# Kernel tuning notes

Measured on AMD Instinct MI355X. Metric: run time of the kernel, lower is better.

Reference implementation:

```python
import jax, jax.numpy as jnp
import numpy as np

H = 32        # query heads
KVH = 8       # key/value heads
D = 64        # head_dim
HID = 2048
B, S = 2, 2048

def rotate_half(x):
    x1, x2 = x[..., :D // 2], x[..., D // 2:]
    return jnp.concatenate((-x2, x1), axis=-1)

def setup_inputs() -> dict:
    key = jax.random.key(0)
    ks = jax.random.split(key, 7)
    scale = 1.0 / np.sqrt(HID)
    return {
        "x": jax.random.normal(ks[0], (B, S, HID), jnp.float32),
        "cos": jax.random.uniform(ks[1], (S, D), jnp.float32),
        "sin": jax.random.uniform(ks[2], (S, D), jnp.float32),
        "wq": jax.random.normal(ks[3], (HID, H * D), jnp.float32) * scale,
        "wk": jax.random.normal(ks[4], (HID, KVH * D), jnp.float32) * scale,
        "wv": jax.random.normal(ks[5], (HID, KVH * D), jnp.float32) * scale,
        "wo": jax.random.normal(ks[6], (HID, HID), jnp.float32) * scale,
    }

def reference(x, cos, sin, wq, wk, wv, wo):
    b, s, _ = x.shape
    # QKV projections -> [b, heads, s, d]
    q = (x @ wq).reshape(b, s, H, D).transpose(0, 2, 1, 3)
    k = (x @ wk).reshape(b, s, KVH, D).transpose(0, 2, 1, 3)
    v = (x @ wv).reshape(b, s, KVH, D).transpose(0, 2, 1, 3)
    # RoPE (cos/sin broadcast over batch and heads)
    c = cos[None, None, :, :]
    si = sin[None, None, :, :]
    q = q * c + rotate_half(q) * si
    k = k * c + rotate_half(k) * si
    # GQA: expand kv heads (repeat_interleave on head axis)
    g = H // KVH
    k = jnp.repeat(k, g, axis=1)
    v = jnp.repeat(v, g, axis=1)
    # causal SDPA
    scores = jnp.einsum("bhqd,bhkd->bhqk", q, k) / np.sqrt(D).astype(np.float32)
    causal = jnp.tril(jnp.ones((s, s), dtype=bool))
    scores = jnp.where(causal[None, None], scores, jnp.finfo(scores.dtype).min)
    attn = jax.nn.softmax(scores, axis=-1)
    out = jnp.einsum("bhqk,bhkd->bhqd", attn, v)
    out = out.transpose(0, 2, 1, 3).reshape(b, s, H * D)
    return out @ wo
```

## Files before the change

kernel.cpp:

```cpp
#include <hip/hip_runtime.h>
#include <stdint.h>

#define B_ 2
#define S_ 2048
#define H_ 32
#define KVH_ 8
#define D_ 64
#define HID_ 2048

typedef float f32x4 __attribute__((ext_vector_type(4)));
typedef float f32x16 __attribute__((ext_vector_type(16)));
typedef short bf16x8 __attribute__((ext_vector_type(8)));
typedef unsigned short u16;
typedef unsigned short u16x4 __attribute__((ext_vector_type(4)));
typedef unsigned short u16x8 __attribute__((ext_vector_type(8)));
typedef unsigned int u32;
typedef unsigned int u32x2 __attribute__((ext_vector_type(2)));
typedef unsigned int u32x4 __attribute__((ext_vector_type(4)));

__device__ __forceinline__ u16 f2b(float f) {
  unsigned u = __builtin_bit_cast(unsigned, f);
  u += 0x7fffu + ((u >> 16) & 1u);
  return (u16)(u >> 16);
}
__device__ __forceinline__ float b2f(u16 h) {
  unsigned u = ((unsigned)h) << 16;
  return __builtin_bit_cast(float, u);
}
__device__ __forceinline__ void gl_lds16(const void* g, void* l) {
  __builtin_amdgcn_global_load_lds(
      (const __attribute__((address_space(1))) unsigned*)g,
      (__attribute__((address_space(3))) unsigned*)l, 16, 0, 0);
}
__device__ __forceinline__ f32x4 mfma16(bf16x8 a, bf16x8 b, f32x4 c) {
  return __builtin_amdgcn_mfma_f32_16x16x32_bf16(a, b, c, 0, 0, 0);
}
__device__ __forceinline__ f32x16 mfma32(bf16x8 a, bf16x8 b, f32x16 c) {
  return __builtin_amdgcn_mfma_f32_32x32x16_bf16(a, b, c, 0, 0, 0);
}
__device__ __forceinline__ u32 cvtpk(float lo, float hi) {
  u32 r;
  asm("v_cvt_pk_bf16_f32 %0, %1, %2" : "=v"(r) : "v"(lo), "v"(hi));
  return r;
}
__device__ __forceinline__ float fast_exp2(float x) {
#if __has_builtin(__builtin_amdgcn_exp2f)
  return __builtin_amdgcn_exp2f(x);
#else
  return exp2f(x);
#endif
}
__device__ __forceinline__ void swap32(u32 a, u32 b, u32& x, u32& y) {
#if __has_builtin(__builtin_amdgcn_permlane32_swap)
  auto r = __builtin_amdgcn_permlane32_swap(a, b, false, false);
  x = r[0];
  y = r[1];
#else
  u32 sa = (u32)__shfl_xor((int)a, 32), sb = (u32)__shfl_xor((int)b, 32);
  bool hib = (threadIdx.x & 32) != 0;
  x = hib ? sb : a;
  y = hib ? b : sa;
#endif
}

__global__ __launch_bounds__(256) void k_cvt(const float* __restrict__ src,
                                             u16* __restrict__ dst, int n4) {
  int i = blockIdx.x * 256 + threadIdx.x;
  if (i >= n4) return;
  f32x4 v = *(const f32x4*)(src + (size_t)i * 4);
  u16x4 o;
  o[0] = f2b(v[0]); o[1] = f2b(v[1]); o[2] = f2b(v[2]); o[3] = f2b(v[3]);
  *(u16x4*)(dst + (size_t)i * 4) = o;
}

__global__ __launch_bounds__(256) void k_transpose4(const float* __restrict__ wq,
                                                    const float* __restrict__ wk,
                                                    const float* __restrict__ wv,
                                                    const float* __restrict__ wo,
                                                    u16* __restrict__ wqkvT,
                                                    u16* __restrict__ woT) {
  __shared__ float t[32][33];
  const int K = 2048;
  int bx = blockIdx.x;
  const float* src;
  u16* dst;
  int N, n0;
  if (bx < 64) {
    src = wq; dst = wqkvT; N = 2048; n0 = bx * 32;
  } else if (bx < 80) {
    src = wk; dst = wqkvT + (size_t)2048 * 2048; N = 512; n0 = (bx - 64) * 32;
  } else if (bx < 96) {
    src = wv; dst = wqkvT + (size_t)2560 * 2048; N = 512; n0 = (bx - 80) * 32;
  } else {
    src = wo; dst = woT; N = 2048; n0 = (bx - 96) * 32;
  }
  int k0 = blockIdx.y * 32;
  int tt = threadIdx.x;
  int r = tt >> 3, c4 = (tt & 7) << 2;
  f32x4 v = *(const f32x4*)(src + (size_t)(k0 + r) * N + n0 + c4);
  t[r][c4 + 0] = v[0]; t[r][c4 + 1] = v[1];
  t[r][c4 + 2] = v[2]; t[r][c4 + 3] = v[3];
  __syncthreads();
  u16x4 o;
  o[0] = f2b(t[c4 + 0][r]); o[1] = f2b(t[c4 + 1][r]);
  o[2] = f2b(t[c4 + 2][r]); o[3] = f2b(t[c4 + 3][r]);
  *(u16x4*)(dst + (size_t)(n0 + r) * K + k0 + c4) = o;
}

__device__ __forceinline__ void stage64(const u16* __restrict__ G, int rowbase,
                                        int K, int kt, u16* unit, int tid) {
  int r = tid >> 3, sl = tid & 7;
  gl_lds16(G + (size_t)(rowbase + r) * K + kt * 64 + ((sl ^ (r & 7)) << 3),
           (char*)unit + tid * 16);
}

template <int BN, int OUTF32>
__global__ __launch_bounds__(512, 1) void k_gemm8(const u16* __restrict__ A,
                                                  const u16* __restrict__ BT,
                                                  float* __restrict__ Cf,
                                                  u16* __restrict__ Cb,
                                                  int M, int N, int K) {
  constexpr int ATILE = 256 * 64;
  constexpr int BTILE = BN * 64;
  constexpr int BU = BN / 64;
  constexpr int WN = (BN == 128) ? 2 : 4;
  constexpr int NI = (BN == 192) ? 3 : 4;
  constexpr int MI = (BN == 128) ? 4 : 8;
  constexpr int MIP = MI / 4;
  __shared__ __align__(16) u16 sm[2 * ATILE + 2 * BTILE];
  const int tid = threadIdx.x;
  const int l = tid & 63;
  const int lg = (l >> 4) & 3, lr = l & 15;
  const int w = tid >> 6;
  const int wm = w / WN, wn = w % WN;

  const int nwg = gridDim.x;
  const int cpx = nwg >> 3;
  const int bid = blockIdx.x;
  const int swz = (bid & 7) * cpx + (bid >> 3);
  const int ntn = N / BN;
  const int bm = swz / ntn, bn = swz % ntn;
  const int m0 = bm << 8, n0 = bn * BN;

  const u16* Ag = A + (size_t)m0 * K;
  const u16* Bg = BT + (size_t)n0 * K;
  u16* As = sm;
  u16* Bs = sm + 2 * ATILE;

  const int nt = K >> 6;
  f32x4 acc[MI][NI] = {};

#pragma unroll
  for (int u = 0; u < 4; ++u) stage64(Ag, u * 64, K, 0, As + u * 4096, tid);
#pragma unroll
  for (int u = 0; u < BU; ++u) stage64(Bg, u * 64, K, 0, Bs + u * 4096, tid);
  stage64(Ag, 0, K, 1, As + ATILE, tid);
  stage64(Ag, 64, K, 1, As + ATILE + 4096, tid);
  asm volatile("s_waitcnt vmcnt(2)" ::: "memory");
  __builtin_amdgcn_s_barrier();
  asm volatile("" ::: "memory");

  for (int t = 0; t < nt; ++t) {
    const int cur = t & 1;
    u16* Ac = As + cur * ATILE;
    u16* Bc = Bs + cur * BTILE;
    u16* An = As + (cur ^ 1) * ATILE;
    u16* Bn = Bs + (cur ^ 1) * BTILE;
    bf16x8 bc[NI][2];
#pragma unroll
    for (int q = 0; q < 4; ++q) {
      bf16x8 af[MIP][2];
#pragma unroll
      for (int mi2 = 0; mi2 < MIP; ++mi2)
#pragma unroll
        for (int ks = 0; ks < 2; ++ks) {
          int row = wm * (MI * 16) + (q * MIP + mi2) * 16 + lr;
          int slot = (ks * 4 + lg) ^ (lr & 7);
          af[mi2][ks] = *(const bf16x8*)&Ac[row * 64 + slot * 8];
        }
      if (q == 0) {
#pragma unroll
        for (int ni = 0; ni < NI; ++ni)
#pragma unroll
          for (int ks = 0; ks < 2; ++ks) {
            int row = wn * (NI * 16) + ni * 16 + lr;
            int slot = (ks * 4 + lg) ^ (lr & 7);
            bc[ni][ks] = *(const bf16x8*)&Bc[row * 64 + slot * 8];
          }
      }
      if (t + 1 < nt) {
        if (q == 0) {
          stage64(Ag, 128, K, t + 1, An + 2 * 4096, tid);
          stage64(Ag, 192, K, t + 1, An + 3 * 4096, tid);
        } else if (q == 1) {
          stage64(Bg, 0, K, t + 1, Bn, tid);
          stage64(Bg, 64, K, t + 1, Bn + 4096, tid);
        } else if (q == 2) {
          if (BU >= 3) stage64(Bg, 128, K, t + 1, Bn + 2 * 4096, tid);
          if (BU >= 4) stage64(Bg, 192, K, t + 1, Bn + 3 * 4096, tid);
        }
      }
      __builtin_amdgcn_s_barrier();
      asm volatile("" ::: "memory");
      __builtin_amdgcn_s_setprio(1);
#pragma unroll
      for (int mi2 = 0; mi2 < MIP; ++mi2)
#pragma unroll
        for (int ni = 0; ni < NI; ++ni)
#pragma unroll
          for (int ks = 0; ks < 2; ++ks)
            acc[q * MIP + mi2][ni] =
                mfma16(af[mi2][ks], bc[ni][ks], acc[q * MIP + mi2][ni]);
      __builtin_amdgcn_s_setprio(0);
      if (q == 3) {
        if (t + 2 < nt) {
          stage64(Ag, 0, K, t + 2, Ac, tid);
          stage64(Ag, 64, K, t + 2, Ac + 4096, tid);
          asm volatile("s_waitcnt vmcnt(2)" ::: "memory");
        } else if (t + 1 < nt) {
          asm volatile("s_waitcnt vmcnt(0)" ::: "memory");
        }
      }
      __builtin_amdgcn_s_barrier();
      asm volatile("" ::: "memory");
    }
  }

#pragma unroll
  for (int mi = 0; mi < MI; ++mi)
#pragma unroll
    for (int ni = 0; ni < NI; ++ni)
#pragma unroll
      for (int j = 0; j < 4; ++j) {
        size_t row = (size_t)m0 + wm * (MI * 16) + mi * 16 + lg * 4 + j;
        size_t col = (size_t)n0 + wn * (NI * 16) + ni * 16 + lr;
        if (OUTF32)
          Cf[row * N + col] = acc[mi][ni][j];
        else
          Cb[row * N + col] = f2b(acc[mi][ni][j]);
      }
}

__global__ __launch_bounds__(256) void k_rope(const u16* __restrict__ qkv,
                                              const float* __restrict__ cosb,
                                              const float* __restrict__ sinb,
                                              u16* __restrict__ Kr) {
  int task = blockIdx.x * 16 + (threadIdx.x >> 4);
  int t16 = threadIdx.x & 15;
  int kvh = task & 7;
  int row = task >> 3;
  int b = row >> 11, s = row & (S_ - 1);
  int d2 = t16 * 2;
  const u16* base = qkv + (size_t)row * 3072 + 2048 + kvh * 64;
  u32 lo = *(const u32*)(base + d2);
  u32 hi = *(const u32*)(base + d2 + 32);
  float xl0 = b2f((u16)lo), xl1 = b2f((u16)(lo >> 16));
  float xh0 = b2f((u16)hi), xh1 = b2f((u16)(hi >> 16));
  const float* cb = cosb + s * 64;
  const float* sb = sinb + s * 64;
  float cl0 = cb[d2], cl1 = cb[d2 + 1], ch0 = cb[d2 + 32], ch1 = cb[d2 + 33];
  float sl0 = sb[d2], sl1 = sb[d2 + 1], sh0 = sb[d2 + 32], sh1 = sb[d2 + 33];
  float ol0 = xl0 * cl0 - xh0 * sl0;
  float ol1 = xl1 * cl1 - xh1 * sl1;
  float oh0 = xh0 * ch0 + xl0 * sh0;
  float oh1 = xh1 * ch1 + xl1 * sh1;
  u16* dst = Kr + ((size_t)(b * KVH_ + kvh) * S_ + s) * 64;
  *(u32*)(dst + d2) = (u32)f2b(ol0) | ((u32)f2b(ol1) << 16);
  *(u32*)(dst + d2 + 32) = (u32)f2b(oh0) | ((u32)f2b(oh1) << 16);
}

__global__ __launch_bounds__(256) void k_vtrans(const u16* __restrict__ qkv,
                                                u16* __restrict__ Vt) {
  int bid = blockIdx.x;
  int st = bid & 31, kvh = (bid >> 5) & 7, b = bid >> 8;
  int s0 = st * 64;
  __shared__ u16 t[64][72];
  int tid = threadIdx.x;
  int sl = tid >> 2, c16 = (tid & 3) << 4;
  const u16* src = qkv + (size_t)(b * S_ + s0 + sl) * 3072 + 2560 + kvh * 64 + c16;
  u16x8 v0 = *(const u16x8*)src;
  u16x8 v1 = *(const u16x8*)(src + 8);
#pragma unroll
  for (int i = 0; i < 8; ++i) { t[sl][c16 + i] = v0[i]; t[sl][c16 + 8 + i] = v1[i]; }
  __syncthreads();
  int dl = tid >> 2, s16 = (tid & 3) << 4;
  u16x8 o0, o1;
#pragma unroll
  for (int i = 0; i < 8; ++i) { o0[i] = t[s16 + i][dl]; o1[i] = t[s16 + 8 + i][dl]; }
  u16* dst = Vt + ((size_t)(b * KVH_ + kvh) * 64 + dl) * S_ + s0 + s16;
  *(u16x8*)dst = o0;
  *(u16x8*)(dst + 8) = o1;
}

__device__ __forceinline__ void stage_kv8(const u16* __restrict__ Kg,
                                          const u16* __restrict__ Vg, int k0,
                                          u16* ldsK, u16* ldsV, int tid) {
  int r = tid >> 3, cc = tid & 7;
  gl_lds16(Kg + (size_t)(k0 + r) * 64 + ((cc ^ (r & 7)) << 3), ldsK + tid * 8);
  gl_lds16(Vg + (size_t)r * S_ + k0 + ((cc ^ (r & 7)) << 3), ldsV + tid * 8);
}

__device__ __forceinline__ void repack2(const f32x16 s, bf16x8& f0, bf16x8& f1) {
  bf16x8 outv[2];
#pragma unroll
  for (int h = 0; h < 2; ++h) {
    u32 a0 = cvtpk(s[8 * h + 0], s[8 * h + 1]);
    u32 a1 = cvtpk(s[8 * h + 4], s[8 * h + 5]);
    u32 b0 = cvtpk(s[8 * h + 2], s[8 * h + 3]);
    u32 b1 = cvtpk(s[8 * h + 6], s[8 * h + 7]);
    u32 x0, y0, x1, y1;
    swap32(a0, a1, x0, y0);
    swap32(b0, b1, x1, y1);
    u32x4 t;
    t[0] = x0; t[1] = x1; t[2] = y0; t[3] = y1;
    outv[h] = __builtin_bit_cast(bf16x8, t);
  }
  f0 = outv[0];
  f1 = outv[1];
}

__global__ __launch_bounds__(512) void k_attn(const u16* __restrict__ qkv,
                                              const u16* __restrict__ Kr,
                                              const u16* __restrict__ Vt,
                                              const float* __restrict__ cosb,
                                              const float* __restrict__ sinb,
                                              u16* __restrict__ Oout) {
  __shared__ __align__(16) u16 lds[16384];
  const int tid = threadIdx.x;
  const int w = tid >> 6, l = tid & 63;
  const int hi = l >> 5, l31 = l & 31;

  const int bid = blockIdx.x;
  const int g = bid >> 6;
  const int qtl = (g < 4) ? (7 - g) : (g - 4);
  const int hh = (bid >> 1) & 31;
  const int b = bid & 1;
  const int kvh = hh >> 2;
  const int q0 = qtl * 256;
  const int qw0 = q0 + w * 32;
  const int nt = 4 * qtl + 4;

  int off8[4];
#pragma unroll
  for (int c = 0; c < 4; ++c)
    off8[c] = l31 * 64 + ((((c << 1) | hi) ^ (l31 & 7)) << 3);

  const int s_q = qw0 + l31;
  const u16* qsrc = qkv + (size_t)(b * S_ + s_q) * 3072 + hh * 64;
  bf16x8 qf[4];
  {
    const float* cb = cosb + s_q * 64;
    const float* sb = sinb + s_q * 64;
#pragma unroll
    for (int cp = 0; cp < 2; ++cp) {
      bf16x8 rlo = *(const bf16x8*)(qsrc + cp * 16 + hi * 8);
      bf16x8 rhi = *(const bf16x8*)(qsrc + 32 + cp * 16 + hi * 8);
      int dlo = cp * 16 + hi * 8;
      float ol[8], oh[8];
#pragma unroll
      for (int j = 0; j < 8; ++j) {
        float ql = b2f((u16)rlo[j]), qh = b2f((u16)rhi[j]);
        ol[j] = (ql * cb[dlo + j] - qh * sb[dlo + j]) * 0.18033688f;
        oh[j] = (qh * cb[dlo + 32 + j] + ql * sb[dlo + 32 + j]) * 0.18033688f;
      }
      u32x4 plo, phi;
#pragma unroll
      for (int j2 = 0; j2 < 4; ++j2) {
        plo[j2] = cvtpk(ol[2 * j2], ol[2 * j2 + 1]);
        phi[j2] = cvtpk(oh[2 * j2], oh[2 * j2 + 1]);
      }
      qf[cp] = __builtin_bit_cast(bf16x8, plo);
      qf[cp + 2] = __builtin_bit_cast(bf16x8, phi);
    }
  }

  const u16* Kg = Kr + (size_t)(b * KVH_ + kvh) * S_ * 64;
  const u16* Vg = Vt + (size_t)(b * KVH_ + kvh) * 64 * S_;

  f32x16 o0 = {}, o1 = {};
  float l_run = 0.f;

  stage_kv8(Kg, Vg, 0, lds, lds + 4096, tid);
  asm volatile("s_waitcnt vmcnt(0)" ::: "memory");
  __builtin_amdgcn_s_barrier();
  asm volatile("" ::: "memory");

  for (int kt = 0; kt < nt; ++kt) {
    const int cur = kt & 1;
    const int k0 = kt * 64;
    if (kt + 1 < nt)
      stage_kv8(Kg, Vg, k0 + 64, lds + (cur ^ 1) * 8192,
                lds + (cur ^ 1) * 8192 + 4096, tid);

    if (k0 <= qw0 + 31) {
      const u16* Kc = lds + cur * 8192;
      const u16* Vc = Kc + 4096;

      f32x16 sl = {}, sh = {};
      __builtin_amdgcn_s_setprio(1);
#pragma unroll
      for (int c = 0; c < 4; ++c) {
        bf16x8 klo = *(const bf16x8*)(Kc + off8[c]);
        bf16x8 khi = *(const bf16x8*)(Kc + 2048 + off8[c]);
        sl = mfma32(klo, qf[c], sl);
        sh = mfma32(khi, qf[c], sh);
      }
      __builtin_amdgcn_s_setprio(0);

      if (k0 + 63 > qw0) {
        int qg = qw0 + l31;
#pragma unroll
        for (int r = 0; r < 16; ++r) {
          int kg = k0 + (r & 3) + 8 * (r >> 2) + 4 * hi;
          if (kg > qg) sl[r] = -3e38f;
          if (kg + 32 > qg) sh[r] = -3e38f;
        }
      }

      float smv[16];
#pragma unroll
      for (int i = 0; i < 16; ++i) {
        sl[i] = fast_exp2(sl[i]);
        sh[i] = fast_exp2(sh[i]);
        smv[i] = sl[i] + sh[i];
      }
#pragma unroll
      for (int i = 0; i < 8; ++i) smv[i] += smv[i + 8];
#pragma unroll
      for (int i = 0; i < 4; ++i) smv[i] += smv[i + 4];
      smv[0] = (smv[0] + smv[2]) + (smv[1] + smv[3]);
      l_run += smv[0] + __shfl_xor(smv[0], 32);

      bf16x8 pf[4];
      repack2(sl, pf[0], pf[1]);
      repack2(sh, pf[2], pf[3]);

      __builtin_amdgcn_s_setprio(1);
#pragma unroll
      for (int sub = 0; sub < 4; ++sub) {
        bf16x8 v0 = *(const bf16x8*)(Vc + off8[sub]);
        bf16x8 v1 = *(const bf16x8*)(Vc + 2048 + off8[sub]);
        o0 = mfma32(v0, pf[sub], o0);
        o1 = mfma32(v1, pf[sub], o1);
      }
      __builtin_amdgcn_s_setprio(0);
    }

    asm volatile("s_waitcnt vmcnt(0)" ::: "memory");
    __builtin_amdgcn_s_barrier();
    asm volatile("" ::: "memory");
  }

  {
    u16* ep = lds + w * 2048;
    float inv = 1.0f / l_run;
    float oc[32];
#pragma unroll
    for (int i = 0; i < 16; ++i) { oc[i] = o0[i]; oc[16 + i] = o1[i]; }
#pragma unroll
    for (int dh = 0; dh < 2; ++dh)
#pragma unroll
      for (int g2 = 0; g2 < 4; ++g2) {
        u32 w0 = cvtpk(oc[dh * 16 + 4 * g2 + 0] * inv, oc[dh * 16 + 4 * g2 + 1] * inv);
        u32 w1 = cvtpk(oc[dh * 16 + 4 * g2 + 2] * inv, oc[dh * 16 + 4 * g2 + 3] * inv);
        int col = dh * 32 + 8 * g2 + 4 * hi;
        u32x2 tw; tw[0] = w0; tw[1] = w1;
        *(u32x2*)&ep[l31 * 64 + col] = tw;
      }
    asm volatile("s_waitcnt lgkmcnt(0)" ::: "memory");
    int row = l >> 1;
    size_t gb = ((size_t)(b * S_ + q0 + w * 32 + row)) * HID_ + hh * 64 + (l & 1) * 32;
#pragma unroll
    for (int cc = 0; cc < 4; ++cc) {
      u16x8 v = *(const u16x8*)&ep[row * 64 + (l & 1) * 32 + cc * 8];
      *(u16x8*)&Oout[gb + cc * 8] = v;
    }
  }
}

extern "C" void kernel_launch(void* const* d_in, const int* in_sizes, int n_in,
                              void* d_out, int out_size, void* d_ws, size_t ws_size,
                              hipStream_t stream) {
  (void)in_sizes; (void)n_in; (void)out_size; (void)ws_size;
  const float* x    = (const float*)d_in[0];
  const float* cosb = (const float*)d_in[1];
  const float* sinb = (const float*)d_in[2];
  const float* wq   = (const float*)d_in[3];
  const float* wk   = (const float*)d_in[4];
  const float* wv   = (const float*)d_in[5];
  const float* wo   = (const float*)d_in[6];

  char* wsb = (char*)d_ws;
  u16* xb    = (u16*)(wsb + 0);
  u16* wqkvT = (u16*)(wsb + 16777216);
  u16* woT   = (u16*)(wsb + 29360128);
  u16* qkv   = (u16*)(wsb + 37748736);
  u16* attno = (u16*)(wsb + 62914560);
  u16* Kr    = (u16*)(wsb + 79691776);
  u16* Vt    = (u16*)(wsb + 83886080);

  k_cvt<<<8192, 256, 0, stream>>>(x, xb, (B_ * S_ * HID_) / 4);
  k_transpose4<<<dim3(160, 64), 256, 0, stream>>>(wq, wk, wv, wo, wqkvT, woT);

  k_gemm8<192, 0><<<256, 512, 0, stream>>>(xb, wqkvT, nullptr, qkv, 4096, 3072, 2048);

  k_rope<<<2048, 256, 0, stream>>>(qkv, cosb, sinb, Kr);
  k_vtrans<<<512, 256, 0, stream>>>(qkv, Vt);

  k_attn<<<512, 512, 0, stream>>>(qkv, Kr, Vt, cosb, sinb, attno);

  k_gemm8<128, 1><<<256, 512, 0, stream>>>(attno, woT, (float*)d_out, nullptr,
                                           4096, 2048, 2048);
}
```

Before: 175.1 us.

## Triple-buffer B tiles and halve per-K-step barrier phases in GEMM

```diff
diff --git a/kernel.cpp b/kernel.cpp
--- a/kernel.cpp
+++ b/kernel.cpp
@@ -126,8 +126,8 @@
   constexpr int WN = (BN == 128) ? 2 : 4;
   constexpr int NI = (BN == 192) ? 3 : 4;
   constexpr int MI = (BN == 128) ? 4 : 8;
-  constexpr int MIP = MI / 4;
-  __shared__ __align__(16) u16 sm[2 * ATILE + 2 * BTILE];
+  constexpr int MIH = MI / 2;
+  __shared__ __align__(16) u16 sm[2 * ATILE + 3 * BTILE];
   const int tid = threadIdx.x;
   const int l = tid & 63;
   const int lg = (l >> 4) & 3, lr = l & 15;
@@ -150,81 +150,111 @@
   const int nt = K >> 6;
   f32x4 acc[MI][NI] = {};
 
+#define VMCNT_KEEP()                                          \
+  do {                                                        \
+    if constexpr (BU == 2)                                    \
+      asm volatile("s_waitcnt vmcnt(4)" ::: "memory");        \
+    else if constexpr (BU == 3)                               \
+      asm volatile("s_waitcnt vmcnt(5)" ::: "memory");        \
+    else                                                      \
+      asm volatile("s_waitcnt vmcnt(6)" ::: "memory");        \
+  } while (0)
+
 #pragma unroll
   for (int u = 0; u < 4; ++u) stage64(Ag, u * 64, K, 0, As + u * 4096, tid);
 #pragma unroll
   for (int u = 0; u < BU; ++u) stage64(Bg, u * 64, K, 0, Bs + u * 4096, tid);
   stage64(Ag, 0, K, 1, As + ATILE, tid);
   stage64(Ag, 64, K, 1, As + ATILE + 4096, tid);
-  asm volatile("s_waitcnt vmcnt(2)" ::: "memory");
+#pragma unroll
+  for (int u = 0; u < BU; ++u)
+    stage64(Bg, u * 64, K, 1, Bs + BTILE + u * 4096, tid);
+  VMCNT_KEEP();
   __builtin_amdgcn_s_barrier();
   asm volatile("" ::: "memory");
 
   for (int t = 0; t < nt; ++t) {
-    const int cur = t & 1;
-    u16* Ac = As + cur * ATILE;
-    u16* Bc = Bs + cur * BTILE;
-    u16* An = As + (cur ^ 1) * ATILE;
-    u16* Bn = Bs + (cur ^ 1) * BTILE;
+    u16* Ac = As + (t & 1) * ATILE;
+    u16* Bc = Bs + (t % 3) * BTILE;
+    u16* An = As + ((t + 1) & 1) * ATILE;
+    u16* Bn2 = Bs + ((t + 2) % 3) * BTILE;
     bf16x8 bc[NI][2];
-#pragma unroll
-    for (int q = 0; q < 4; ++q) {
-      bf16x8 af[MIP][2];
-#pragma unroll
-      for (int mi2 = 0; mi2 < MIP; ++mi2)
-#pragma unroll
-        for (int ks = 0; ks < 2; ++ks) {
-          int row = wm * (MI * 16) + (q * MIP + mi2) * 16 + lr;
-          int slot = (ks * 4 + lg) ^ (lr & 7);
-          af[mi2][ks] = *(const bf16x8*)&Ac[row * 64 + slot * 8];
-        }
-      if (q == 0) {
-#pragma unroll
-        for (int ni = 0; ni < NI; ++ni)
-#pragma unroll
-          for (int ks = 0; ks < 2; ++ks) {
-            int row = wn * (NI * 16) + ni * 16 + lr;
-            int slot = (ks * 4 + lg) ^ (lr & 7);
-            bc[ni][ks] = *(const bf16x8*)&Bc[row * 64 + slot * 8];
-          }
-      }
-      if (t + 1 < nt) {
-        if (q == 0) {
-          stage64(Ag, 128, K, t + 1, An + 2 * 4096, tid);
-          stage64(Ag, 192, K, t + 1, An + 3 * 4096, tid);
-        } else if (q == 1) {
-          stage64(Bg, 0, K, t + 1, Bn, tid);
-          stage64(Bg, 64, K, t + 1, Bn + 4096, tid);
-        } else if (q == 2) {
-          if (BU >= 3) stage64(Bg, 128, K, t + 1, Bn + 2 * 4096, tid);
-          if (BU >= 4) stage64(Bg, 192, K, t + 1, Bn + 3 * 4096, tid);
-        }
-      }
-      __builtin_amdgcn_s_barrier();
-      asm volatile("" ::: "memory");
-      __builtin_amdgcn_s_setprio(1);
-#pragma unroll
-      for (int mi2 = 0; mi2 < MIP; ++mi2)
-#pragma unroll
-        for (int ni = 0; ni < NI; ++ni)
-#pragma unroll
-          for (int ks = 0; ks < 2; ++ks)
-            acc[q * MIP + mi2][ni] =
-                mfma16(af[mi2][ks], bc[ni][ks], acc[q * MIP + mi2][ni]);
-      __builtin_amdgcn_s_setprio(0);
-      if (q == 3) {
-        if (t + 2 < nt) {
-          stage64(Ag, 0, K, t + 2, Ac, tid);
-          stage64(Ag, 64, K, t + 2, Ac + 4096, tid);
-          asm volatile("s_waitcnt vmcnt(2)" ::: "memory");
-        } else if (t + 1 < nt) {
-          asm volatile("s_waitcnt vmcnt(0)" ::: "memory");
-        }
-      }
-      __builtin_amdgcn_s_barrier();
-      asm volatile("" ::: "memory");
-    }
+
+    bf16x8 af0[MIH][2];
+#pragma unroll
+    for (int mi2 = 0; mi2 < MIH; ++mi2)
+#pragma unroll
+      for (int ks = 0; ks < 2; ++ks) {
+        int row = wm * (MI * 16) + mi2 * 16 + lr;
+        int slot = (ks * 4 + lg) ^ (lr & 7);
+        af0[mi2][ks] = *(const bf16x8*)&Ac[row * 64 + slot * 8];
+      }
+#pragma unroll
+    for (int ni = 0; ni < NI; ++ni)
+#pragma unroll
+      for (int ks = 0; ks < 2; ++ks) {
+        int row = wn * (NI * 16) + ni * 16 + lr;
+        int slot = (ks * 4 + lg) ^ (lr & 7);
+        bc[ni][ks] = *(const bf16x8*)&Bc[row * 64 + slot * 8];
+      }
+    if (t + 1 < nt) {
+      stage64(Ag, 128, K, t + 1, An + 2 * 4096, tid);
+      stage64(Ag, 192, K, t + 1, An + 3 * 4096, tid);
+    }
+    if (t + 2 < nt) {
+      stage64(Bg, 0, K, t + 2, Bn2, tid);
+      stage64(Bg, 64, K, t + 2, Bn2 + 4096, tid);
+    }
+    __builtin_amdgcn_s_barrier();
+    asm volatile("" ::: "memory");
+    __builtin_amdgcn_s_setprio(1);
+#pragma unroll
+    for (int mi2 = 0; mi2 < MIH; ++mi2)
+#pragma unroll
+      for (int ni = 0; ni < NI; ++ni)
+#pragma unroll
+        for (int ks = 0; ks < 2; ++ks)
+          acc[mi2][ni] = mfma16(af0[mi2][ks], bc[ni][ks], acc[mi2][ni]);
+    __builtin_amdgcn_s_setprio(0);
+    __builtin_amdgcn_s_barrier();
+    asm volatile("" ::: "memory");
+
+    bf16x8 af1[MIH][2];
+#pragma unroll
+    for (int mi2 = 0; mi2 < MIH; ++mi2)
+#pragma unroll
+      for (int ks = 0; ks < 2; ++ks) {
+        int row = wm * (MI * 16) + (MIH + mi2) * 16 + lr;
+        int slot = (ks * 4 + lg) ^ (lr & 7);
+        af1[mi2][ks] = *(const bf16x8*)&Ac[row * 64 + slot * 8];
+      }
+    if (t + 2 < nt) {
+      if (BU >= 3) stage64(Bg, 128, K, t + 2, Bn2 + 2 * 4096, tid);
+      if (BU >= 4) stage64(Bg, 192, K, t + 2, Bn2 + 3 * 4096, tid);
+    }
+    __builtin_amdgcn_s_barrier();
+    asm volatile("" ::: "memory");
+    __builtin_amdgcn_s_setprio(1);
+#pragma unroll
+    for (int mi2 = 0; mi2 < MIH; ++mi2)
+#pragma unroll
+      for (int ni = 0; ni < NI; ++ni)
+#pragma unroll
+        for (int ks = 0; ks < 2; ++ks)
+          acc[MIH + mi2][ni] =
+              mfma16(af1[mi2][ks], bc[ni][ks], acc[MIH + mi2][ni]);
+    __builtin_amdgcn_s_setprio(0);
+    if (t + 2 < nt) {
+      stage64(Ag, 0, K, t + 2, Ac, tid);
+      stage64(Ag, 64, K, t + 2, Ac + 4096, tid);
+      VMCNT_KEEP();
+    } else if (t + 1 < nt) {
+      asm volatile("s_waitcnt vmcnt(0)" ::: "memory");
+    }
+    __builtin_amdgcn_s_barrier();
+    asm volatile("" ::: "memory");
   }
+#undef VMCNT_KEEP
 
 #pragma unroll
   for (int mi = 0; mi < MI; ++mi)
```

Measured after the change: 175.6 us. No clear change (+0.2%).
